# Optimization experiments

Measured on AMD Instinct MI355X. Metric: run time of the kernel, lower is better.

## Reference

```python
import jax, jax.numpy as jnp
import numpy as np

# init kwargs baked in as constants
VTH_M = 0.5
VTH_S = 0.1
DECAY_M = 2.0
DECAY_S = 0.1
ALPHA = 4.0

B, T, C, H, W = 16, 32, 64, 32, 32


def spike_fn(x):
    # Heaviside spike; forward only (surrogate gradient used in bwd module)
    return jnp.where(x > 0, 1.0, 0.0).astype(x.dtype)


def setup_inputs() -> dict:
    key = jax.random.key(0)
    k1, k2, k3 = jax.random.split(key, 3)
    x = jax.random.normal(k1, (B, T, C, H, W), dtype=jnp.float32)
    vth_raw = jax.random.normal(k2, (C, H, W), dtype=jnp.float32)
    decay_raw = jax.random.normal(k3, (C, H, W), dtype=jnp.float32)
    return {"x": x, "vth_raw": vth_raw, "decay_raw": decay_raw}


def reference(x, vth_raw, decay_raw):
    # learned per-neuron threshold and decay
    vth = jax.nn.softplus(vth_raw * VTH_S + VTH_M) + 0.01          # (C,H,W)
    decay = jnp.clip(jax.nn.sigmoid(decay_raw * DECAY_S + DECAY_M), 0.0, 0.99)

    x_seq = jnp.moveaxis(x, 1, 0)  # (T, B, C, H, W)

    def scan_fn(v, x_t):
        v = v * decay + x_t                      # leaky integrate
        s = spike_fn(v - vth)                    # fire
        v = v - jax.lax.stop_gradient(s) * vth   # soft reset
        return v, s

    _, spikes = jax.lax.scan(scan_fn, jnp.zeros_like(x_seq[0]), x_seq)
    return jnp.moveaxis(spikes, 0, 1)  # (B, T, C, H, W)
```

## Files before the change

kernel.cpp:

```cpp
#include <hip/hip_runtime.h>
#include <math.h>


#define LIF_B   16
#define LIF_T   32
#define LIF_CHW 65536
#define LIF_CHW4 16384

__global__ __launch_bounds__(256) void HR_HLIFLayer2D_kernel(
    const float* __restrict__ x,
    const float* __restrict__ vth_raw,
    const float* __restrict__ decay_raw,
    float* __restrict__ out)
{
    const int g = blockIdx.x * 256 + threadIdx.x;
    const int b = g >> 14;
    const int j = g & (LIF_CHW4 - 1);

    const float4 vr4 = reinterpret_cast<const float4*>(vth_raw)[j];
    const float4 dr4 = reinterpret_cast<const float4*>(decay_raw)[j];
    const float vrr[4] = {vr4.x, vr4.y, vr4.z, vr4.w};
    const float drr[4] = {dr4.x, dr4.y, dr4.z, dr4.w};

    float vth[4], dec[4];
#pragma unroll
    for (int i = 0; i < 4; ++i) {
        float a  = __fmul_rn(vrr[i], 0.1f);
        float bb = __fadd_rn(a, 0.5f);
        double sp = log1p(exp((double)bb));
        vth[i] = __fadd_rn((float)sp, 0.01f);

        float z = __fmul_rn(drr[i], 0.1f);
        float w = __fadd_rn(z, 2.0f);
        double sg = 1.0 / (1.0 + exp(-(double)w));
        float sgf = (float)sg;
        sgf = fminf(fmaxf(sgf, 0.0f), 0.99f);
        dec[i] = sgf;
    }

    float v[4] = {0.f, 0.f, 0.f, 0.f};
    const size_t base4 = (size_t)b * (LIF_T * LIF_CHW4) + (size_t)j;
    const float4* __restrict__ x4 = reinterpret_cast<const float4*>(x);
    float4* __restrict__ o4 = reinterpret_cast<float4*>(out);

#pragma unroll
    for (int t = 0; t < LIF_T; ++t) {
        const size_t idx = base4 + (size_t)t * LIF_CHW4;
        const float4 xt = x4[idx];
        const float xi[4] = {xt.x, xt.y, xt.z, xt.w};
        float s[4];
#pragma unroll
        for (int i = 0; i < 4; ++i) {
            float vv = __fadd_rn(__fmul_rn(v[i], dec[i]), xi[i]);
            float d = __fsub_rn(vv, vth[i]);
            bool fire = (d > 0.0f);
            s[i] = fire ? 1.0f : 0.0f;
            v[i] = fire ? d : vv;
        }
        o4[idx] = make_float4(s[0], s[1], s[2], s[3]);
    }
}

extern "C" void kernel_launch(void* const* d_in, const int* in_sizes, int n_in,
                              void* d_out, int out_size, void* d_ws, size_t ws_size,
                              hipStream_t stream) {
    const float* x         = (const float*)d_in[0];
    const float* vth_raw   = (const float*)d_in[1];
    const float* decay_raw = (const float*)d_in[2];
    float* out             = (float*)d_out;

    const int total_threads = LIF_B * LIF_CHW4;
    const int block = 256;
    const int grid = total_threads / block;
    HR_HLIFLayer2D_kernel<<<grid, block, 0, stream>>>(x, vth_raw, decay_raw, out);
}
```

Baseline: 240.7 us.

## Use float2 per thread, prefetch next timestep, nontemporal spike stores

Each thread now handles two neurons with float2 loads instead of four with float4, which doubles the thread count to 512K and should raise occupancy and memory-level parallelism. The next timestep's input is loaded one step ahead of its use, a software prefetch that overlaps the load with the current step's update. Output spikes are written with nontemporal stores to avoid polluting the cache. In exchange, each memory access is narrower and the double-precision parameter setup is repeated over twice as many threads.

```diff
diff --git a/kernel.cpp b/kernel.cpp
--- a/kernel.cpp
+++ b/kernel.cpp
@@ -2,10 +2,12 @@
 #include <math.h>
 
 
-#define LIF_B   16
-#define LIF_T   32
-#define LIF_CHW 65536
-#define LIF_CHW4 16384
+#define LIF_B    16
+#define LIF_T    32
+#define LIF_CHW  65536
+#define LIF_CHW2 32768
+
+typedef float vf2 __attribute__((ext_vector_type(2)));
 
 __global__ __launch_bounds__(256) void HR_HLIFLayer2D_kernel(
     const float* __restrict__ x,
@@ -14,17 +16,17 @@
     float* __restrict__ out)
 {
     const int g = blockIdx.x * 256 + threadIdx.x;
-    const int b = g >> 14;
-    const int j = g & (LIF_CHW4 - 1);
+    const int b = g >> 15;
+    const int j = g & (LIF_CHW2 - 1);
 
-    const float4 vr4 = reinterpret_cast<const float4*>(vth_raw)[j];
-    const float4 dr4 = reinterpret_cast<const float4*>(decay_raw)[j];
-    const float vrr[4] = {vr4.x, vr4.y, vr4.z, vr4.w};
-    const float drr[4] = {dr4.x, dr4.y, dr4.z, dr4.w};
+    const vf2 vr2 = reinterpret_cast<const vf2*>(vth_raw)[j];
+    const vf2 dr2 = reinterpret_cast<const vf2*>(decay_raw)[j];
+    const float vrr[2] = {vr2.x, vr2.y};
+    const float drr[2] = {dr2.x, dr2.y};
 
-    float vth[4], dec[4];
+    float vth[2], dec[2];
 #pragma unroll
-    for (int i = 0; i < 4; ++i) {
+    for (int i = 0; i < 2; ++i) {
         float a  = __fmul_rn(vrr[i], 0.1f);
         float bb = __fadd_rn(a, 0.5f);
         double sp = log1p(exp((double)bb));
@@ -38,26 +40,32 @@
         dec[i] = sgf;
     }
 
-    float v[4] = {0.f, 0.f, 0.f, 0.f};
-    const size_t base4 = (size_t)b * (LIF_T * LIF_CHW4) + (size_t)j;
-    const float4* __restrict__ x4 = reinterpret_cast<const float4*>(x);
-    float4* __restrict__ o4 = reinterpret_cast<float4*>(out);
+    float v[2] = {0.f, 0.f};
+    const size_t base2 = (size_t)b * (LIF_T * LIF_CHW2) + (size_t)j;
+    const vf2* __restrict__ x2 = reinterpret_cast<const vf2*>(x);
+    vf2* __restrict__ o2 = reinterpret_cast<vf2*>(out);
 
+    vf2 xt = x2[base2];
 #pragma unroll
     for (int t = 0; t < LIF_T; ++t) {
-        const size_t idx = base4 + (size_t)t * LIF_CHW4;
-        const float4 xt = x4[idx];
-        const float xi[4] = {xt.x, xt.y, xt.z, xt.w};
-        float s[4];
+        const size_t idx = base2 + (size_t)t * LIF_CHW2;
+        vf2 xn;
+        if (t + 1 < LIF_T) xn = x2[idx + LIF_CHW2];
+
+        const float xi[2] = {xt.x, xt.y};
+        vf2 s;
+        float so[2];
 #pragma unroll
-        for (int i = 0; i < 4; ++i) {
+        for (int i = 0; i < 2; ++i) {
             float vv = __fadd_rn(__fmul_rn(v[i], dec[i]), xi[i]);
             float d = __fsub_rn(vv, vth[i]);
             bool fire = (d > 0.0f);
-            s[i] = fire ? 1.0f : 0.0f;
+            so[i] = fire ? 1.0f : 0.0f;
             v[i] = fire ? d : vv;
         }
-        o4[idx] = make_float4(s[0], s[1], s[2], s[3]);
+        s.x = so[0]; s.y = so[1];
+        __builtin_nontemporal_store(s, &o2[idx]);
+        xt = xn;
     }
 }
 
@@ -69,7 +77,7 @@
     const float* decay_raw = (const float*)d_in[2];
     float* out             = (float*)d_out;
 
-    const int total_threads = LIF_B * LIF_CHW4;
+    const int total_threads = LIF_B * LIF_CHW2;
     const int block = 256;
     const int grid = total_threads / block;
     HR_HLIFLayer2D_kernel<<<grid, block, 0, stream>>>(x, vth_raw, decay_raw, out);
```

Result: faster. 232.7 us (-3.3%).
